# Kernel optimization log

Hardware: AMD Instinct MI355X
Metric: run time of the kernel (lower is better)

Reference implementation:

```python
import jax, jax.numpy as jnp
import numpy as np

A_BIT = 4
W_BIT = 4
IN_PLANES = 32
OUT_PLANES = 32
EXPANSION = 6
PLANES = EXPANSION * IN_PLANES  # 192


def _fake_quant(x, bits):
    """Per-tensor symmetric fake quantization to `bits` (round + clip, dequantized)."""
    qmax = 2.0 ** (bits - 1) - 1.0
    scale = jnp.maximum(jnp.max(jnp.abs(x)) / qmax, 1e-8)
    y = x / scale
    # straight-through round
    yq = jnp.clip(y + jax.lax.stop_gradient(jnp.round(y) - y), -qmax - 1.0, qmax)
    return yq * scale


def _conv(x, w, stride=1, padding=0, groups=1):
    return jax.lax.conv_general_dilated(
        x, w,
        window_strides=(stride, stride),
        padding=[(padding, padding), (padding, padding)],
        dimension_numbers=("NCHW", "OIHW", "NCHW"),
        feature_group_count=groups,
    )


def _qconv(x, w, stride=1, padding=0, groups=1):
    # FuseConv2dQ: fake-quantize activation (a_bit) and weight (w_bit), then fp conv
    return _conv(_fake_quant(x, A_BIT), _fake_quant(w, W_BIT),
                 stride=stride, padding=padding, groups=groups)


def setup_inputs() -> dict:
    key = jax.random.key(0)
    k0, k1, k2, k3 = jax.random.split(key, 4)
    x = jax.random.normal(k0, (32, IN_PLANES, 112, 112), dtype=jnp.float32)
    # conv1: 1x1 expand  [planes, in_planes, 1, 1]
    w1 = jax.random.normal(k1, (PLANES, IN_PLANES, 1, 1), dtype=jnp.float32) * 0.1
    # conv2: 3x3 depthwise, groups=planes -> [planes, 1, 3, 3]
    w2 = jax.random.normal(k2, (PLANES, 1, 3, 3), dtype=jnp.float32) * 0.1
    # conv3: 1x1 project  [out_planes, planes, 1, 1]
    w3 = jax.random.normal(k3, (OUT_PLANES, PLANES, 1, 1), dtype=jnp.float32) * 0.1
    return {"x": x, "w1": w1, "w2": w2, "w3": w3}


def reference(x, w1, w2, w3):
    out = jax.nn.relu(_qconv(x, w1))                                   # expand 1x1
    out = jax.nn.relu(_qconv(out, w2, stride=1, padding=1, groups=PLANES))  # depthwise 3x3
    out = _qconv(out, w3)                                              # project 1x1
    # stride == 1 and in_planes == out_planes -> identity shortcut
    return out + x
```

## Files before the change

kernel.cpp:

```cpp
#include <hip/hip_runtime.h>

#define NB   32
#define CIN  32
#define PL   192
#define CP   96
#define NG1  4
#define NG3  24
#define HH   112
#define WID  112
#define HW   12544
#define COUT 32
#define SEGS 784
#define PXB  1568
#define SEG8 14
#define RT8  784

#define W2NOFF 64
#define W1NOFF (W2NOFF + CP*8)
#define W3NOFF (W1NOFF + NG1*PL)
#define Q1OFF_BYTES 65536
#define QBYTES ((size_t)NB*CP*HW)

__device__ __forceinline__ int sdot8(unsigned int a, unsigned int b, int c) {
#if defined(__has_builtin) && __has_builtin(__builtin_amdgcn_sdot8)
  return __builtin_amdgcn_sdot8((int)a, (int)b, c, false);
#else
#pragma unroll
  for (int i = 0; i < 8; ++i)
    c += ((int)(a << (28 - 4 * i)) >> 28) * ((int)(b << (28 - 4 * i)) >> 28);
  return c;
#endif
}

template <int SH>
__device__ __forceinline__ unsigned int winsh(unsigned int hi, unsigned int lo) {
#if defined(__has_builtin) && __has_builtin(__builtin_amdgcn_perm)
  const unsigned int sel = (SH == 1) ? 0x04030201u : (SH == 2) ? 0x05040302u : 0x06050403u;
  return __builtin_amdgcn_perm(hi, lo, sel);
#else
  return (lo >> (8 * SH)) | (hi << (32 - 8 * SH));
#endif
}

__device__ __forceinline__ float quant87(float v, float s) {
  return fminf(fmaxf(rintf(v / s), -8.0f), 7.0f);
}

__device__ __forceinline__ void block_max_commit(int lmax, int* __restrict__ slot) {
  __shared__ int red[4];
  for (int o = 32; o; o >>= 1) lmax = max(lmax, __shfl_down(lmax, o));
  if ((threadIdx.x & 63) == 0) red[threadIdx.x >> 6] = lmax;
  __syncthreads();
  if (threadIdx.x == 0) {
    int m = max(max(red[0], red[1]), max(red[2], red[3]));
    int cur = *(const volatile int*)slot;
    if (m > cur) atomicMax(slot, m);
  }
}

__global__ void kzero(int* __restrict__ wsi) {
  if (threadIdx.x < 16) wsi[threadIdx.x] = 0;
}

__global__ void kmax_all(const float* __restrict__ x, int n4,
                         const float* __restrict__ w1, const float* __restrict__ w2,
                         const float* __restrict__ w3, int* __restrict__ wsi) {
  float m = 0.f;
  int slot;
  if (blockIdx.x < 1024) {
    const float4* x4 = (const float4*)x;
    for (int i = blockIdx.x * blockDim.x + threadIdx.x; i < n4; i += 1024 * blockDim.x) {
      float4 v = x4[i];
      m = fmaxf(fmaxf(fabsf(v.x), fabsf(v.y)), fmaxf(fmaxf(fabsf(v.z), fabsf(v.w)), m));
    }
    slot = 0;
  } else {
    const float* p; int n;
    int w = blockIdx.x - 1024;
    if (w == 0)      { p = w1; n = PL * CIN; }
    else if (w == 1) { p = w2; n = PL * 9; }
    else             { p = w3; n = COUT * PL; }
    for (int i = threadIdx.x; i < n; i += blockDim.x) m = fmaxf(m, fabsf(p[i]));
    slot = 1 + w;
  }
  block_max_commit(__float_as_int(m), wsi + slot);
}

__global__ void kprep(const float* __restrict__ w1, const float* __restrict__ w2,
                      const float* __restrict__ w3, float* __restrict__ wsf) {
  int* wsi = (int*)wsf;
  unsigned int* wsu = (unsigned int*)wsf;
  __shared__ float ss[4];
  if (threadIdx.x == 0) {
    float sx  = fmaxf(__int_as_float(wsi[0]) / 7.0f, 1e-8f);
    float sw1 = fmaxf(__int_as_float(wsi[1]) / 7.0f, 1e-8f);
    float sw2 = fmaxf(__int_as_float(wsi[2]) / 7.0f, 1e-8f);
    float sw3 = fmaxf(__int_as_float(wsi[3]) / 7.0f, 1e-8f);
    wsf[8] = sx; wsf[9] = sw1; wsf[10] = sw2; wsf[11] = sw3;
    ss[1] = sw1; ss[2] = sw2; ss[3] = sw3;
  }
  __syncthreads();
  float sw1 = ss[1], sw2 = ss[2], sw3 = ss[3];
  for (int i = threadIdx.x; i < NG1 * PL; i += blockDim.x) {
    int g = i / PL, o = i - g * PL;
    unsigned int wrd = 0;
    for (int k = 0; k < 8; ++k)
      wrd |= ((unsigned)((int)quant87(w1[o * CIN + 8 * g + k], sw1) & 15)) << (4 * k);
    wsu[W1NOFF + i] = wrd;
  }
  for (int cp = threadIdx.x; cp < CP; cp += blockDim.x) {
    unsigned int d[8];
    for (int R = 0; R < 3; ++R) {
      int a0 = (int)quant87(w2[(2 * cp) * 9 + 3 * R],     sw2) & 15;
      int a1 = (int)quant87(w2[(2 * cp) * 9 + 3 * R + 1], sw2) & 15;
      int a2 = (int)quant87(w2[(2 * cp) * 9 + 3 * R + 2], sw2) & 15;
      int b0 = (int)quant87(w2[(2 * cp + 1) * 9 + 3 * R],     sw2) & 15;
      int b1 = (int)quant87(w2[(2 * cp + 1) * 9 + 3 * R + 1], sw2) & 15;
      int b2 = (int)quant87(w2[(2 * cp + 1) * 9 + 3 * R + 2], sw2) & 15;
      d[2 * R]     = (unsigned)(a0 | (a1 << 8) | (a2 << 16));
      d[2 * R + 1] = (unsigned)((b0 << 4) | (b1 << 12) | (b2 << 20));
    }
    d[6] = 0u; d[7] = 0u;
    unsigned int* dst = wsu + W2NOFF + cp * 8;
    for (int k = 0; k < 8; ++k) dst[k] = d[k];
  }
  for (int i = threadIdx.x; i < NG3 * COUT; i += blockDim.x) {
    int g = i / COUT, o = i - g * COUT;
    unsigned int wrd = 0;
    for (int k = 0; k < 8; ++k)
      wrd |= ((unsigned)((int)quant87(w3[o * PL + 8 * g + k], sw3) & 15)) << (4 * k);
    wsu[W3NOFF + i] = wrd;
  }
}

__launch_bounds__(256)
__global__ void kquantx(const float* __restrict__ x, const float* __restrict__ wsf,
                        unsigned int* __restrict__ xq4) {
  float sx = wsf[8];
  int t = blockIdx.x * 256 + threadIdx.x;
  int s = t % SEGS;
  int g = (t / SEGS) & 3;
  int n = t / (SEGS * 4);
  const float* xb = x + ((size_t)n * CIN + 8 * g) * HW + s * 16;
  unsigned int* dst = xq4 + ((size_t)n * NG1 + g) * HW + s * 16;
#pragma unroll
  for (int c4 = 0; c4 < 4; ++c4) {
    unsigned int w[4] = {0u, 0u, 0u, 0u};
#pragma unroll
    for (int k = 0; k < 8; ++k) {
      float4 v = *(const float4*)(xb + (size_t)k * HW + c4 * 4);
      w[0] |= ((unsigned)((int)quant87(v.x, sx) & 15)) << (4 * k);
      w[1] |= ((unsigned)((int)quant87(v.y, sx) & 15)) << (4 * k);
      w[2] |= ((unsigned)((int)quant87(v.z, sx) & 15)) << (4 * k);
      w[3] |= ((unsigned)((int)quant87(v.w, sx) & 15)) << (4 * k);
    }
    uint4 o; o.x = w[0]; o.y = w[1]; o.z = w[2]; o.w = w[3];
    *(uint4*)(dst + c4 * 4) = o;
  }
}

template <int STORE>
__launch_bounds__(256)
__global__ void kconv1(const unsigned int* __restrict__ xq4, const float* __restrict__ wsf,
                       unsigned char* __restrict__ q1, int* __restrict__ maxslot) {
  __shared__ unsigned int lw[NG1 * 64];
  __shared__ unsigned char lut[2176];
  const int* wsi = (const int*)wsf;
  const unsigned int* wsu = (const unsigned int*)wsf;
  int ogb = blockIdx.x / PXB;
  int pxb = blockIdx.x - ogb * PXB;
  {
    int g = threadIdx.x >> 6, ol = threadIdx.x & 63;
    lw[threadIdx.x] = wsu[W1NOFF + g * PL + ogb * 64 + ol];
  }
  if (STORE) {
    float S1 = wsf[8] * wsf[9];
    float sh1 = fmaxf((S1 * (float)wsi[4]) / 7.0f, 1e-8f);
    for (int i = threadIdx.x; i < 2176; i += 256)
      lut[i] = (unsigned char)fminf(rintf((S1 * (float)i) / sh1), 7.0f);
  }
  __syncthreads();
  int og = threadIdx.x >> 5;
  int pxl = threadIdx.x & 31;
  int gp = pxb * 256 + pxl * 8;
  int n = gp / HW, pos = gp - n * HW;
  const unsigned int* xw = xq4 + (size_t)n * NG1 * HW + pos;
  int acc[8][8] = {};
#pragma unroll
  for (int g = 0; g < NG1; ++g) {
    uint4 xa = *(const uint4*)(xw + (size_t)g * HW);
    uint4 xb = *(const uint4*)(xw + (size_t)g * HW + 4);
    uint4 wa = *(const uint4*)&lw[g * 64 + og * 8];
    uint4 wb = *(const uint4*)&lw[g * 64 + og * 8 + 4];
    unsigned int xv[8] = {xa.x, xa.y, xa.z, xa.w, xb.x, xb.y, xb.z, xb.w};
    unsigned int wv[8] = {wa.x, wa.y, wa.z, wa.w, wb.x, wb.y, wb.z, wb.w};
#pragma unroll
    for (int o = 0; o < 8; ++o)
#pragma unroll
      for (int j = 0; j < 8; ++j)
        acc[o][j] = sdot8(xv[j], wv[o], acc[o][j]);
  }
  if (!STORE) {
    int lmax = 0;
#pragma unroll
    for (int o = 0; o < 8; ++o)
#pragma unroll
      for (int j = 0; j < 8; ++j)
        lmax = max(lmax, max(acc[o][j], 0));
    block_max_commit(lmax, maxslot);
  } else {
    int cpb = ogb * 32 + og * 4;
#pragma unroll
    for (int m = 0; m < 4; ++m) {
      unsigned int b0 = 0, b1 = 0;
#pragma unroll
      for (int j = 0; j < 4; ++j) {
        int i0 = max(acc[2 * m][j], 0);
        int i1 = max(acc[2 * m + 1][j], 0);
        b0 |= ((unsigned)(lut[i0] | (lut[i1] << 4))) << (8 * j);
        int i2 = max(acc[2 * m][4 + j], 0);
        int i3 = max(acc[2 * m + 1][4 + j], 0);
        b1 |= ((unsigned)(lut[i2] | (lut[i3] << 4))) << (8 * j);
      }
      uint2 w; w.x = b0; w.y = b1;
      *(uint2*)(q1 + ((size_t)n * CP + cpb + m) * HW + pos) = w;
    }
  }
}

template <int STORE>
__launch_bounds__(256)
__global__ void kconv2(const unsigned char* __restrict__ q1, const float* __restrict__ wsf,
                       unsigned int* __restrict__ q2w, int* __restrict__ maxslot) {
  const int* wsi = (const int*)wsf;
  const unsigned int* w2n = (const unsigned int*)wsf + W2NOFF;
  __shared__ unsigned char lut[1024];
  if (STORE) {
    float S1 = wsf[8] * wsf[9];
    float sh1 = fmaxf((S1 * (float)wsi[4]) / 7.0f, 1e-8f);
    float S2 = sh1 * wsf[10];
    float sh2 = fmaxf((S2 * (float)wsi[5]) / 7.0f, 1e-8f);
    for (int i = threadIdx.x; i < 1024; i += 256) {
      int a = i - 512;
      lut[i] = (a <= 0) ? (unsigned char)0
                        : (unsigned char)fminf(rintf((S2 * (float)a) / sh2), 7.0f);
    }
    __syncthreads();
  }
  int gid = blockIdx.x * 256 + threadIdx.x;
  int nG = gid / RT8;
  int t  = gid - nG * RT8;
  int r2 = t / SEG8;
  int c  = t - r2 * SEG8;
  int y0 = r2 * 2, x0 = c * 8;
  int n = nG / NG3, G = nG - n * NG3;
  int cp0 = G * 4;
  const unsigned char* base = q1 + ((size_t)n * CP + cp0) * HW + x0;
  int rofs[4]; bool rok[4];
#pragma unroll
  for (int R = 0; R < 4; ++R) {
    int yy = y0 - 1 + R;
    rok[R] = (unsigned)yy < (unsigned)HH;
    rofs[R] = min(max(yy, 0), HH - 1) * WID;
  }
  bool has_l = (c > 0), has_r = (c < SEG8 - 1);
  unsigned int wacc[16];
  if (STORE) {
#pragma unroll
    for (int j = 0; j < 16; ++j) wacc[j] = 0u;
  }
  int lmax = 0;
#pragma unroll
  for (int p = 0; p < 4; ++p) {
    unsigned int wc0[3], wc1[3];
    {
      const unsigned int* wp = w2n + (size_t)(cp0 + p) * 8;
      uint4 wa = *(const uint4*)wp;
      uint2 wb = *(const uint2*)(wp + 4);
      wc0[0] = wa.x; wc1[0] = wa.y; wc0[1] = wa.z; wc1[1] = wa.w;
      wc0[2] = wb.x; wc1[2] = wb.y;
    }
    const unsigned char* pb = base + (size_t)p * HW;
    int a0r0[8] = {}, a1r0[8] = {}, a0r1[8] = {}, a1r1[8] = {};
#pragma unroll
    for (int R = 0; R < 4; ++R) {
      const unsigned char* rp = pb + rofs[R];
      uint2 u = *(const uint2*)rp;
      unsigned int lwr = *(const unsigned int*)(rp - 4);
      unsigned int rwr = *(const unsigned int*)(rp + 8);
      u.x = rok[R] ? u.x : 0u;
      u.y = rok[R] ? u.y : 0u;
      lwr = (rok[R] && has_l) ? lwr : 0u;
      rwr = (rok[R] && has_r) ? rwr : 0u;
      unsigned int W[8];
      W[0] = winsh<3>(u.x, lwr);
      W[1] = u.x;
      W[2] = winsh<1>(u.y, u.x);
      W[3] = winsh<2>(u.y, u.x);
      W[4] = winsh<3>(u.y, u.x);
      W[5] = u.y;
      W[6] = winsh<1>(rwr, u.y);
      W[7] = winsh<2>(rwr, u.y);
      if (R <= 2) {
#pragma unroll
        for (int j = 0; j < 8; ++j) {
          a0r0[j] = sdot8(W[j], wc0[R], a0r0[j]);
          a1r0[j] = sdot8(W[j], wc1[R], a1r0[j]);
        }
      }
      if (R >= 1) {
#pragma unroll
        for (int j = 0; j < 8; ++j) {
          a0r1[j] = sdot8(W[j], wc0[R - 1], a0r1[j]);
          a1r1[j] = sdot8(W[j], wc1[R - 1], a1r1[j]);
        }
      }
    }
    if (!STORE) {
#pragma unroll
      for (int j = 0; j < 8; ++j) {
        lmax = max(lmax, max(a0r0[j], a1r0[j]));
        lmax = max(lmax, max(a0r1[j], a1r1[j]));
      }
    } else {
#pragma unroll
      for (int j = 0; j < 8; ++j) {
        unsigned int b0 = (unsigned)lut[512 + a0r0[j]] | ((unsigned)lut[512 + a1r0[j]] << 4);
        unsigned int b1 = (unsigned)lut[512 + a0r1[j]] | ((unsigned)lut[512 + a1r1[j]] << 4);
        wacc[j]     |= b0 << (8 * p);
        wacc[8 + j] |= b1 << (8 * p);
      }
    }
  }
  if (!STORE) {
    block_max_commit(max(lmax, 0), maxslot);
  } else {
    unsigned int* d0 = q2w + (size_t)nG * HW + (size_t)y0 * WID + x0;
    unsigned int* d1 = d0 + WID;
    uint4 o;
    o.x = wacc[0]; o.y = wacc[1]; o.z = wacc[2]; o.w = wacc[3];
    *(uint4*)d0 = o;
    o.x = wacc[4]; o.y = wacc[5]; o.z = wacc[6]; o.w = wacc[7];
    *(uint4*)(d0 + 4) = o;
    o.x = wacc[8]; o.y = wacc[9]; o.z = wacc[10]; o.w = wacc[11];
    *(uint4*)d1 = o;
    o.x = wacc[12]; o.y = wacc[13]; o.z = wacc[14]; o.w = wacc[15];
    *(uint4*)(d1 + 4) = o;
  }
}

__launch_bounds__(256)
__global__ void kconv3(const unsigned int* __restrict__ q2w, const float* __restrict__ x,
                       const float* __restrict__ wsf, float* __restrict__ out) {
  __shared__ unsigned int lw[NG3 * COUT];
  const unsigned int* wsu = (const unsigned int*)wsf;
  for (int i = threadIdx.x; i < NG3 * COUT; i += 256) lw[i] = wsu[W3NOFF + i];
  const int* wsi = (const int*)wsf;
  float S1 = wsf[8] * wsf[9];
  float sh1 = fmaxf((S1 * (float)wsi[4]) / 7.0f, 1e-8f);
  float S2 = sh1 * wsf[10];
  float sh2 = fmaxf((S2 * (float)wsi[5]) / 7.0f, 1e-8f);
  float S3 = sh2 * wsf[11];
  __syncthreads();
  int og = threadIdx.x >> 6;
  int lane = threadIdx.x & 63;
  int gp = blockIdx.x * 256 + lane * 4;
  int n = gp / HW, pos = gp - n * HW;
  const unsigned int* qp = q2w + (size_t)n * NG3 * HW + pos;
  int acc[8][4] = {};
#pragma unroll 4
  for (int g = 0; g < NG3; ++g) {
    uint4 qv = *(const uint4*)(qp + (size_t)g * HW);
    uint4 wa = *(const uint4*)&lw[g * COUT + og * 8];
    uint4 wb = *(const uint4*)&lw[g * COUT + og * 8 + 4];
    unsigned int pv[4] = {qv.x, qv.y, qv.z, qv.w};
    unsigned int wv[8] = {wa.x, wa.y, wa.z, wa.w, wb.x, wb.y, wb.z, wb.w};
#pragma unroll
    for (int o = 0; o < 8; ++o)
#pragma unroll
      for (int j = 0; j < 4; ++j)
        acc[o][j] = sdot8(pv[j], wv[o], acc[o][j]);
  }
  int ob = og * 8;
#pragma unroll
  for (int o = 0; o < 8; ++o) {
    const float* xp = x + ((size_t)n * COUT + ob + o) * HW + pos;
    float* op = out + ((size_t)n * COUT + ob + o) * HW + pos;
    float4 xv = *(const float4*)xp;
    float4 r;
    r.x = fmaf(S3, (float)acc[o][0], xv.x);
    r.y = fmaf(S3, (float)acc[o][1], xv.y);
    r.z = fmaf(S3, (float)acc[o][2], xv.z);
    r.w = fmaf(S3, (float)acc[o][3], xv.w);
    *(float4*)op = r;
  }
}

extern "C" void kernel_launch(void* const* d_in, const int* in_sizes, int n_in,
                              void* d_out, int out_size, void* d_ws, size_t ws_size,
                              hipStream_t stream) {
  const float* x  = (const float*)d_in[0];
  const float* w1 = (const float*)d_in[1];
  const float* w2 = (const float*)d_in[2];
  const float* w3 = (const float*)d_in[3];
  float* out = (float*)d_out;

  float* wsf = (float*)d_ws;
  int* wsi = (int*)d_ws;
  unsigned char* q1 = (unsigned char*)d_ws + Q1OFF_BYTES;
  unsigned int* q2w = (unsigned int*)(q1 + QBYTES);
  unsigned int* xq4 = (unsigned int*)d_out;

  kzero<<<1, 64, 0, stream>>>(wsi);

  int n4 = in_sizes[0] / 4;
  kmax_all<<<1027, 256, 0, stream>>>(x, n4, w1, w2, w3, wsi);
  kprep<<<1, 256, 0, stream>>>(w1, w2, w3, wsf);
  kquantx<<<NB * NG1 * SEGS / 256, 256, 0, stream>>>(x, wsf, xq4);

  kconv1<0><<<3 * PXB, 256, 0, stream>>>(xq4, wsf, q1, wsi + 4);
  kconv1<1><<<3 * PXB, 256, 0, stream>>>(xq4, wsf, q1, wsi + 4);

  int nblk2 = NB * NG3 * RT8 / 256;
  kconv2<0><<<nblk2, 256, 0, stream>>>(q1, wsf, q2w, wsi + 5);
  kconv2<1><<<nblk2, 256, 0, stream>>>(q1, wsf, q2w, wsi + 5);

  kconv3<<<NB * HW / 256, 256, 0, stream>>>(q2w, x, wsf, out);
}
```

Measured before the change: 160.8 us.

## Fuse x quantization with conv1 max pass and inline weight prep

```diff
diff --git a/kernel.cpp b/kernel.cpp
--- a/kernel.cpp
+++ b/kernel.cpp
@@ -10,14 +10,11 @@
 #define WID  112
 #define HW   12544
 #define COUT 32
-#define SEGS 784
 #define PXB  1568
 #define SEG8 14
 #define RT8  784
 
 #define W2NOFF 64
-#define W1NOFF (W2NOFF + CP*8)
-#define W3NOFF (W1NOFF + NG1*PL)
 #define Q1OFF_BYTES 65536
 #define QBYTES ((size_t)NB*CP*HW)
 
@@ -44,6 +41,10 @@
 
 __device__ __forceinline__ float quant87(float v, float s) {
   return fminf(fmaxf(rintf(v / s), -8.0f), 7.0f);
+}
+
+__device__ __forceinline__ float scl(int bits) {
+  return fmaxf(__int_as_float(bits) / 7.0f, 1e-8f);
 }
 
 __device__ __forceinline__ void block_max_commit(int lmax, int* __restrict__ slot) {
@@ -56,10 +57,6 @@
     int cur = *(const volatile int*)slot;
     if (m > cur) atomicMax(slot, m);
   }
-}
-
-__global__ void kzero(int* __restrict__ wsi) {
-  if (threadIdx.x < 16) wsi[threadIdx.x] = 0;
 }
 
 __global__ void kmax_all(const float* __restrict__ x, int n4,
@@ -86,100 +83,100 @@
   block_max_commit(__float_as_int(m), wsi + slot);
 }
 
-__global__ void kprep(const float* __restrict__ w1, const float* __restrict__ w2,
-                      const float* __restrict__ w3, float* __restrict__ wsf) {
-  int* wsi = (int*)wsf;
-  unsigned int* wsu = (unsigned int*)wsf;
-  __shared__ float ss[4];
-  if (threadIdx.x == 0) {
-    float sx  = fmaxf(__int_as_float(wsi[0]) / 7.0f, 1e-8f);
-    float sw1 = fmaxf(__int_as_float(wsi[1]) / 7.0f, 1e-8f);
-    float sw2 = fmaxf(__int_as_float(wsi[2]) / 7.0f, 1e-8f);
-    float sw3 = fmaxf(__int_as_float(wsi[3]) / 7.0f, 1e-8f);
-    wsf[8] = sx; wsf[9] = sw1; wsf[10] = sw2; wsf[11] = sw3;
-    ss[1] = sw1; ss[2] = sw2; ss[3] = sw3;
-  }
-  __syncthreads();
-  float sw1 = ss[1], sw2 = ss[2], sw3 = ss[3];
-  for (int i = threadIdx.x; i < NG1 * PL; i += blockDim.x) {
+__launch_bounds__(256)
+__global__ void kqx1(const float* __restrict__ x, const float* __restrict__ w1,
+                     const float* __restrict__ w2, int* __restrict__ wsi,
+                     unsigned int* __restrict__ xq4, unsigned int* __restrict__ w2n,
+                     int* __restrict__ maxslot) {
+  __shared__ unsigned int lw[NG1 * PL];
+  float sx  = scl(wsi[0]);
+  float sw1 = scl(wsi[1]);
+#pragma unroll
+  for (int k = 0; k < 3; ++k) {
+    int i = threadIdx.x + k * 256;
     int g = i / PL, o = i - g * PL;
     unsigned int wrd = 0;
-    for (int k = 0; k < 8; ++k)
-      wrd |= ((unsigned)((int)quant87(w1[o * CIN + 8 * g + k], sw1) & 15)) << (4 * k);
-    wsu[W1NOFF + i] = wrd;
-  }
-  for (int cp = threadIdx.x; cp < CP; cp += blockDim.x) {
-    unsigned int d[8];
-    for (int R = 0; R < 3; ++R) {
-      int a0 = (int)quant87(w2[(2 * cp) * 9 + 3 * R],     sw2) & 15;
-      int a1 = (int)quant87(w2[(2 * cp) * 9 + 3 * R + 1], sw2) & 15;
-      int a2 = (int)quant87(w2[(2 * cp) * 9 + 3 * R + 2], sw2) & 15;
-      int b0 = (int)quant87(w2[(2 * cp + 1) * 9 + 3 * R],     sw2) & 15;
-      int b1 = (int)quant87(w2[(2 * cp + 1) * 9 + 3 * R + 1], sw2) & 15;
-      int b2 = (int)quant87(w2[(2 * cp + 1) * 9 + 3 * R + 2], sw2) & 15;
-      d[2 * R]     = (unsigned)(a0 | (a1 << 8) | (a2 << 16));
-      d[2 * R + 1] = (unsigned)((b0 << 4) | (b1 << 12) | (b2 << 20));
-    }
-    d[6] = 0u; d[7] = 0u;
-    unsigned int* dst = wsu + W2NOFF + cp * 8;
-    for (int k = 0; k < 8; ++k) dst[k] = d[k];
-  }
-  for (int i = threadIdx.x; i < NG3 * COUT; i += blockDim.x) {
-    int g = i / COUT, o = i - g * COUT;
+#pragma unroll
+    for (int j = 0; j < 8; ++j)
+      wrd |= ((unsigned)((int)quant87(w1[o * CIN + 8 * g + j], sw1) & 15)) << (4 * j);
+    lw[i] = wrd;
+  }
+  if (blockIdx.x == 0) {
+    float sw2 = scl(wsi[2]);
+    for (int cp = threadIdx.x; cp < CP; cp += 256) {
+      unsigned int d[8];
+      for (int R = 0; R < 3; ++R) {
+        int a0 = (int)quant87(w2[(2 * cp) * 9 + 3 * R],     sw2) & 15;
+        int a1 = (int)quant87(w2[(2 * cp) * 9 + 3 * R + 1], sw2) & 15;
+        int a2 = (int)quant87(w2[(2 * cp) * 9 + 3 * R + 2], sw2) & 15;
+        int b0 = (int)quant87(w2[(2 * cp + 1) * 9 + 3 * R],     sw2) & 15;
+        int b1 = (int)quant87(w2[(2 * cp + 1) * 9 + 3 * R + 1], sw2) & 15;
+        int b2 = (int)quant87(w2[(2 * cp + 1) * 9 + 3 * R + 2], sw2) & 15;
+        d[2 * R]     = (unsigned)(a0 | (a1 << 8) | (a2 << 16));
+        d[2 * R + 1] = (unsigned)((b0 << 4) | (b1 << 12) | (b2 << 20));
+      }
+      d[6] = 0u; d[7] = 0u;
+      for (int k = 0; k < 8; ++k) w2n[cp * 8 + k] = d[k];
+    }
+  }
+  __syncthreads();
+  int gp = blockIdx.x * 256 + threadIdx.x;
+  int n = gp / HW, pos = gp - n * HW;
+  const float* xp = x + (size_t)n * CIN * HW + pos;
+  unsigned int xv[NG1];
+#pragma unroll
+  for (int g = 0; g < NG1; ++g) {
     unsigned int wrd = 0;
-    for (int k = 0; k < 8; ++k)
-      wrd |= ((unsigned)((int)quant87(w3[o * PL + 8 * g + k], sw3) & 15)) << (4 * k);
-    wsu[W3NOFF + i] = wrd;
-  }
+#pragma unroll
+    for (int j = 0; j < 8; ++j) {
+      float v = xp[(size_t)(8 * g + j) * HW];
+      wrd |= ((unsigned)((int)quant87(v, sx) & 15)) << (4 * j);
+    }
+    xv[g] = wrd;
+    xq4[((size_t)n * NG1 + g) * HW + pos] = wrd;
+  }
+  int lmax = 0;
+#pragma unroll 4
+  for (int o = 0; o < PL; o += 4) {
+    uint4 wg0 = *(const uint4*)&lw[o];
+    uint4 wg1 = *(const uint4*)&lw[PL + o];
+    uint4 wg2 = *(const uint4*)&lw[2 * PL + o];
+    uint4 wg3 = *(const uint4*)&lw[3 * PL + o];
+    int a0 = sdot8(xv[3], wg3.x, sdot8(xv[2], wg2.x, sdot8(xv[1], wg1.x, sdot8(xv[0], wg0.x, 0))));
+    int a1 = sdot8(xv[3], wg3.y, sdot8(xv[2], wg2.y, sdot8(xv[1], wg1.y, sdot8(xv[0], wg0.y, 0))));
+    int a2 = sdot8(xv[3], wg3.z, sdot8(xv[2], wg2.z, sdot8(xv[1], wg1.z, sdot8(xv[0], wg0.z, 0))));
+    int a3 = sdot8(xv[3], wg3.w, sdot8(xv[2], wg2.w, sdot8(xv[1], wg1.w, sdot8(xv[0], wg0.w, 0))));
+    lmax = max(lmax, max(max(a0, a1), max(a2, a3)));
+  }
+  block_max_commit(max(lmax, 0), maxslot);
 }
 
 __launch_bounds__(256)
-__global__ void kquantx(const float* __restrict__ x, const float* __restrict__ wsf,
-                        unsigned int* __restrict__ xq4) {
-  float sx = wsf[8];
-  int t = blockIdx.x * 256 + threadIdx.x;
-  int s = t % SEGS;
-  int g = (t / SEGS) & 3;
-  int n = t / (SEGS * 4);
-  const float* xb = x + ((size_t)n * CIN + 8 * g) * HW + s * 16;
-  unsigned int* dst = xq4 + ((size_t)n * NG1 + g) * HW + s * 16;
-#pragma unroll
-  for (int c4 = 0; c4 < 4; ++c4) {
-    unsigned int w[4] = {0u, 0u, 0u, 0u};
-#pragma unroll
-    for (int k = 0; k < 8; ++k) {
-      float4 v = *(const float4*)(xb + (size_t)k * HW + c4 * 4);
-      w[0] |= ((unsigned)((int)quant87(v.x, sx) & 15)) << (4 * k);
-      w[1] |= ((unsigned)((int)quant87(v.y, sx) & 15)) << (4 * k);
-      w[2] |= ((unsigned)((int)quant87(v.z, sx) & 15)) << (4 * k);
-      w[3] |= ((unsigned)((int)quant87(v.w, sx) & 15)) << (4 * k);
-    }
-    uint4 o; o.x = w[0]; o.y = w[1]; o.z = w[2]; o.w = w[3];
-    *(uint4*)(dst + c4 * 4) = o;
-  }
-}
-
-template <int STORE>
-__launch_bounds__(256)
-__global__ void kconv1(const unsigned int* __restrict__ xq4, const float* __restrict__ wsf,
-                       unsigned char* __restrict__ q1, int* __restrict__ maxslot) {
-  __shared__ unsigned int lw[NG1 * 64];
+__global__ void kconv1s(const unsigned int* __restrict__ xq4, const float* __restrict__ w1,
+                        const int* __restrict__ wsi, unsigned char* __restrict__ q1) {
+  __shared__ unsigned int lw[NG1 * PL];
   __shared__ unsigned char lut[2176];
-  const int* wsi = (const int*)wsf;
-  const unsigned int* wsu = (const unsigned int*)wsf;
-  int ogb = blockIdx.x / PXB;
-  int pxb = blockIdx.x - ogb * PXB;
+  float sx  = scl(wsi[0]);
+  float sw1 = scl(wsi[1]);
+#pragma unroll
+  for (int k = 0; k < 3; ++k) {
+    int i = threadIdx.x + k * 256;
+    int g = i / PL, o = i - g * PL;
+    unsigned int wrd = 0;
+#pragma unroll
+    for (int j = 0; j < 8; ++j)
+      wrd |= ((unsigned)((int)quant87(w1[o * CIN + 8 * g + j], sw1) & 15)) << (4 * j);
+    lw[i] = wrd;
+  }
   {
-    int g = threadIdx.x >> 6, ol = threadIdx.x & 63;
-    lw[threadIdx.x] = wsu[W1NOFF + g * PL + ogb * 64 + ol];
-  }
-  if (STORE) {
-    float S1 = wsf[8] * wsf[9];
+    float S1 = sx * sw1;
     float sh1 = fmaxf((S1 * (float)wsi[4]) / 7.0f, 1e-8f);
     for (int i = threadIdx.x; i < 2176; i += 256)
       lut[i] = (unsigned char)fminf(rintf((S1 * (float)i) / sh1), 7.0f);
   }
   __syncthreads();
+  int ogb = blockIdx.x / PXB;
+  int pxb = blockIdx.x - ogb * PXB;
   int og = threadIdx.x >> 5;
   int pxl = threadIdx.x & 31;
   int gp = pxb * 256 + pxl * 8;
@@ -190,8 +187,8 @@
   for (int g = 0; g < NG1; ++g) {
     uint4 xa = *(const uint4*)(xw + (size_t)g * HW);
     uint4 xb = *(const uint4*)(xw + (size_t)g * HW + 4);
-    uint4 wa = *(const uint4*)&lw[g * 64 + og * 8];
-    uint4 wb = *(const uint4*)&lw[g * 64 + og * 8 + 4];
+    uint4 wa = *(const uint4*)&lw[g * PL + ogb * 64 + og * 8];
+    uint4 wb = *(const uint4*)&lw[g * PL + ogb * 64 + og * 8 + 4];
     unsigned int xv[8] = {xa.x, xa.y, xa.z, xa.w, xb.x, xb.y, xb.z, xb.w};
     unsigned int wv[8] = {wa.x, wa.y, wa.z, wa.w, wb.x, wb.y, wb.z, wb.w};
 #pragma unroll
@@ -200,45 +197,34 @@
       for (int j = 0; j < 8; ++j)
         acc[o][j] = sdot8(xv[j], wv[o], acc[o][j]);
   }
-  if (!STORE) {
-    int lmax = 0;
-#pragma unroll
-    for (int o = 0; o < 8; ++o)
-#pragma unroll
-      for (int j = 0; j < 8; ++j)
-        lmax = max(lmax, max(acc[o][j], 0));
-    block_max_commit(lmax, maxslot);
-  } else {
-    int cpb = ogb * 32 + og * 4;
-#pragma unroll
-    for (int m = 0; m < 4; ++m) {
-      unsigned int b0 = 0, b1 = 0;
-#pragma unroll
-      for (int j = 0; j < 4; ++j) {
-        int i0 = max(acc[2 * m][j], 0);
-        int i1 = max(acc[2 * m + 1][j], 0);
-        b0 |= ((unsigned)(lut[i0] | (lut[i1] << 4))) << (8 * j);
-        int i2 = max(acc[2 * m][4 + j], 0);
-        int i3 = max(acc[2 * m + 1][4 + j], 0);
-        b1 |= ((unsigned)(lut[i2] | (lut[i3] << 4))) << (8 * j);
-      }
-      uint2 w; w.x = b0; w.y = b1;
-      *(uint2*)(q1 + ((size_t)n * CP + cpb + m) * HW + pos) = w;
-    }
+  int cpb = ogb * 32 + og * 4;
+#pragma unroll
+  for (int m = 0; m < 4; ++m) {
+    unsigned int b0 = 0, b1 = 0;
+#pragma unroll
+    for (int j = 0; j < 4; ++j) {
+      int i0 = max(acc[2 * m][j], 0);
+      int i1 = max(acc[2 * m + 1][j], 0);
+      b0 |= ((unsigned)(lut[i0] | (lut[i1] << 4))) << (8 * j);
+      int i2 = max(acc[2 * m][4 + j], 0);
+      int i3 = max(acc[2 * m + 1][4 + j], 0);
+      b1 |= ((unsigned)(lut[i2] | (lut[i3] << 4))) << (8 * j);
+    }
+    uint2 w; w.x = b0; w.y = b1;
+    *(uint2*)(q1 + ((size_t)n * CP + cpb + m) * HW + pos) = w;
   }
 }
 
 template <int STORE>
 __launch_bounds__(256)
-__global__ void kconv2(const unsigned char* __restrict__ q1, const float* __restrict__ wsf,
-                       unsigned int* __restrict__ q2w, int* __restrict__ maxslot) {
-  const int* wsi = (const int*)wsf;
-  const unsigned int* w2n = (const unsigned int*)wsf + W2NOFF;
+__global__ void kconv2(const unsigned char* __restrict__ q1, const unsigned int* __restrict__ w2n,
+                       const int* __restrict__ wsi, unsigned int* __restrict__ q2w,
+                       int* __restrict__ maxslot) {
   __shared__ unsigned char lut[1024];
   if (STORE) {
-    float S1 = wsf[8] * wsf[9];
+    float S1 = scl(wsi[0]) * scl(wsi[1]);
     float sh1 = fmaxf((S1 * (float)wsi[4]) / 7.0f, 1e-8f);
-    float S2 = sh1 * wsf[10];
+    float S2 = sh1 * scl(wsi[2]);
     float sh2 = fmaxf((S2 * (float)wsi[5]) / 7.0f, 1e-8f);
     for (int i = threadIdx.x; i < 1024; i += 256) {
       int a = i - 512;
@@ -351,16 +337,25 @@
 
 __launch_bounds__(256)
 __global__ void kconv3(const unsigned int* __restrict__ q2w, const float* __restrict__ x,
-                       const float* __restrict__ wsf, float* __restrict__ out) {
+                       const float* __restrict__ w3, const int* __restrict__ wsi,
+                       float* __restrict__ out) {
   __shared__ unsigned int lw[NG3 * COUT];
-  const unsigned int* wsu = (const unsigned int*)wsf;
-  for (int i = threadIdx.x; i < NG3 * COUT; i += 256) lw[i] = wsu[W3NOFF + i];
-  const int* wsi = (const int*)wsf;
-  float S1 = wsf[8] * wsf[9];
+  float sw3 = scl(wsi[3]);
+#pragma unroll
+  for (int k = 0; k < 3; ++k) {
+    int i = threadIdx.x + k * 256;
+    int g = i / COUT, o = i - g * COUT;
+    unsigned int wrd = 0;
+#pragma unroll
+    for (int j = 0; j < 8; ++j)
+      wrd |= ((unsigned)((int)quant87(w3[o * PL + 8 * g + j], sw3) & 15)) << (4 * j);
+    lw[i] = wrd;
+  }
+  float S1 = scl(wsi[0]) * scl(wsi[1]);
   float sh1 = fmaxf((S1 * (float)wsi[4]) / 7.0f, 1e-8f);
-  float S2 = sh1 * wsf[10];
+  float S2 = sh1 * scl(wsi[2]);
   float sh2 = fmaxf((S2 * (float)wsi[5]) / 7.0f, 1e-8f);
-  float S3 = sh2 * wsf[11];
+  float S3 = sh2 * sw3;
   __syncthreads();
   int og = threadIdx.x >> 6;
   int lane = threadIdx.x & 63;
@@ -405,25 +400,22 @@
   const float* w3 = (const float*)d_in[3];
   float* out = (float*)d_out;
 
-  float* wsf = (float*)d_ws;
   int* wsi = (int*)d_ws;
+  unsigned int* w2n = (unsigned int*)d_ws + W2NOFF;
   unsigned char* q1 = (unsigned char*)d_ws + Q1OFF_BYTES;
   unsigned int* q2w = (unsigned int*)(q1 + QBYTES);
   unsigned int* xq4 = (unsigned int*)d_out;
 
-  kzero<<<1, 64, 0, stream>>>(wsi);
+  hipMemsetAsync(d_ws, 0, 64, stream);
 
   int n4 = in_sizes[0] / 4;
   kmax_all<<<1027, 256, 0, stream>>>(x, n4, w1, w2, w3, wsi);
-  kprep<<<1, 256, 0, stream>>>(w1, w2, w3, wsf);
-  kquantx<<<NB * NG1 * SEGS / 256, 256, 0, stream>>>(x, wsf, xq4);
-
-  kconv1<0><<<3 * PXB, 256, 0, stream>>>(xq4, wsf, q1, wsi + 4);
-  kconv1<1><<<3 * PXB, 256, 0, stream>>>(xq4, wsf, q1, wsi + 4);
+  kqx1<<<PXB, 256, 0, stream>>>(x, w1, w2, wsi, xq4, w2n, wsi + 4);
+  kconv1s<<<3 * PXB, 256, 0, stream>>>(xq4, w1, wsi, q1);
 
   int nblk2 = NB * NG3 * RT8 / 256;
-  kconv2<0><<<nblk2, 256, 0, stream>>>(q1, wsf, q2w, wsi + 5);
-  kconv2<1><<<nblk2, 256, 0, stream>>>(q1, wsf, q2w, wsi + 5);
-
-  kconv3<<<NB * HW / 256, 256, 0, stream>>>(q2w, x, wsf, out);
-}
+  kconv2<0><<<nblk2, 256, 0, stream>>>(q1, w2n, wsi, q2w, wsi + 5);
+  kconv2<1><<<nblk2, 256, 0, stream>>>(q1, w2n, wsi, q2w, wsi + 5);
+
+  kconv3<<<NB * HW / 256, 256, 0, stream>>>(q2w, x, w3, wsi, out);
+}
```

New measurement: 177.5 us. 1.1x slower.
